# Optimization experiments

Hardware: AMD Instinct MI355X
Metric: run time of the kernel (lower is better)

The kernel has to match this reference:

```python
import jax, jax.numpy as jnp
import numpy as np

B, N, CIN, K, HID = 16, 4096, 64, 64, 128
RATIO, RADIUS = 0.25, 0.2
S = int(N * RATIO)  # 1024 sampled centers per cloud


def setup_inputs() -> dict:
    key = jax.random.key(0)
    k1, k2, k3, k4 = jax.random.split(key, 4)
    x = jax.random.normal(k1, (B * N, CIN), jnp.float32)
    pos = jax.random.uniform(k2, (B * N, 3), jnp.float32)  # unit cube
    batch = jnp.repeat(jnp.arange(B, dtype=jnp.int32), N)  # sorted cloud ids
    W1 = jax.random.normal(k3, (CIN + 3, HID), jnp.float32) / np.sqrt(CIN + 3)
    b1 = jnp.zeros((HID,), jnp.float32)
    W2 = jax.random.normal(k4, (HID, HID), jnp.float32) / np.sqrt(HID)
    b2 = jnp.zeros((HID,), jnp.float32)
    return {"x": x, "pos": pos, "batch": batch, "W1": W1, "b1": b1, "W2": W2, "b2": b2}


def _fps(pos_b):
    """Farthest point sampling on one cloud [N,3] -> S int32 indices (start=0, deterministic)."""
    def step(carry, _):
        min_d, last = carry
        d = jnp.sum((pos_b - pos_b[last]) ** 2, axis=-1)  # [N]
        min_d = jnp.minimum(min_d, d)
        nxt = jnp.argmax(min_d).astype(jnp.int32)
        return (min_d, nxt), last
    init = (jnp.full((N,), jnp.inf, pos_b.dtype), jnp.int32(0))
    _, idx = jax.lax.scan(step, init, None, length=S)
    return idx  # [S]


def _forward(x, pos, W1, b1, W2, b2):
    xb = x.reshape(B, N, CIN)
    pb = pos.reshape(B, N, 3)
    idx = jax.vmap(_fps)(pb)  # [B,S]
    centers = jnp.take_along_axis(pb, idx[:, :, None], axis=1)  # [B,S,3]
    # ball query: squared dists centers->all points of same cloud
    d2 = jnp.sum((centers[:, :, None, :] - pb[:, None, :, :]) ** 2, axis=-1)  # [B,S,N]
    masked = jnp.where(d2 <= RADIUS * RADIUS, d2, jnp.inf)
    negv, nbr = jax.lax.top_k(-masked, K)  # K nearest within radius; [B,S,K]
    valid = negv > -jnp.inf  # [B,S,K]
    gather = jax.vmap(lambda a, i: a[i])
    x_j = gather(xb, nbr)  # [B,S,K,CIN]
    p_j = gather(pb, nbr)  # [B,S,K,3]
    rel = p_j - centers[:, :, None, :]
    h = jnp.concatenate([x_j, rel], axis=-1)  # [B,S,K,CIN+3]
    h = jax.nn.relu(h @ W1 + b1)
    h = jax.nn.relu(h @ W2 + b2)  # local_nn message
    h = jnp.where(valid[..., None], h, -jnp.inf)
    out = jnp.max(h, axis=2)  # max-aggregation over neighbors -> [B,S,HID]
    return out.reshape(B * S, HID), centers.reshape(B * S, 3)


def reference(x, pos, batch, W1, b1, W2, b2):
    out, pos_out = _forward(x, pos, W1, b1, W2, b2)
    batch_out = jnp.repeat(jnp.arange(B, dtype=jnp.int32), S)
    return out, pos_out, batch_out
```

## Files before the change

### kernel.cpp

```cpp
#include <hip/hip_runtime.h>
#include <cstdint>
#include <cstddef>

#define BB   16
#define NN   4096
#define CINN 64
#define KKK  64
#define HIDD 128
#define SSS  1024
#define MAXC 320
#define NCH  2
#define CHS  512

typedef __attribute__((ext_vector_type(8))) short short8;
typedef __attribute__((ext_vector_type(4))) float f32x4;
typedef unsigned long long u64;

__device__ __forceinline__ float d2_exact(float ax, float ay, float az,
                                          float bx, float by, float bz) {
  float dx = __fsub_rn(ax, bx);
  float dy = __fsub_rn(ay, by);
  float dz = __fsub_rn(az, bz);
  return __fadd_rn(__fadd_rn(__fmul_rn(dx, dx), __fmul_rn(dy, dy)), __fmul_rn(dz, dz));
}

__device__ __forceinline__ unsigned short f2bf(float f) {
  unsigned u = __float_as_uint(f);
  return (unsigned short)((u + 0x7fffu + ((u >> 16) & 1u)) >> 16);
}

__device__ __forceinline__ void fps_role(int chunk, int bid, int tid,
                                         const float* __restrict__ pos,
                                         int* __restrict__ fps_idx,
                                         float* __restrict__ md_ws,
                                         int* __restrict__ last_ws,
                                         float* __restrict__ pos_out,
                                         float* __restrict__ batch_out,
                                         char* smem) {
  __builtin_amdgcn_s_setprio(3);
  float* px = (float*)smem;
  float* py = px + NN;
  float* pz = py + NN;
  u64* slots = (u64*)(pz + NN);
  int* sel = (int*)(slots + 8);
  const float* pb = pos + (size_t)bid * NN * 3;
  for (int i = tid; i < NN; i += 256) {
    px[i] = pb[3 * i + 0];
    py[i] = pb[3 * i + 1];
    pz[i] = pb[3 * i + 2];
  }
  if (chunk == 0) {
    #pragma unroll
    for (int kk = 0; kk < 4; ++kk)
      batch_out[bid * SSS + kk * 256 + tid] = (float)bid;
  }
  __syncthreads();

  float qx[16], qy[16], qz[16], md[16];
  #pragma unroll
  for (int j = 0; j < 16; ++j) {
    const int i = j * 256 + tid;
    qx[j] = px[i]; qy[j] = py[i]; qz[j] = pz[i];
    asm volatile("" : "+v"(qx[j]), "+v"(qy[j]), "+v"(qz[j]));
    md[j] = __builtin_inff();
  }
  int last, tb;
  const int cbase = chunk * CHS;
  const int te = cbase + CHS;
  if (chunk == 0) {
    last = 0; tb = 1;
    if (tid == 0) {
      fps_idx[bid * SSS] = 0;
      pos_out[(size_t)bid * SSS * 3 + 0] = px[0];
      pos_out[(size_t)bid * SSS * 3 + 1] = py[0];
      pos_out[(size_t)bid * SSS * 3 + 2] = pz[0];
    }
  } else {
    #pragma unroll
    for (int j = 0; j < 16; ++j) md[j] = md_ws[bid * 4096 + j * 256 + tid];
    last = last_ws[bid]; tb = cbase;
  }

  for (int t = tb; t < te; ++t) {
    const float lx = px[last], ly = py[last], lz = pz[last];
    float bv = -1.f;
    int bj = 0;
    #pragma unroll
    for (int j = 0; j < 16; ++j) {
      const float d = d2_exact(qx[j], qy[j], qz[j], lx, ly, lz);
      md[j] = fminf(md[j], d);
      if (md[j] > bv) { bv = md[j]; bj = j; }
    }
    unsigned klo = ~(unsigned)(bj * 256 + tid);
    unsigned khi = __float_as_uint(bv);
#define FPS_DPP_STAGE(CTRL, RMASK)                                                            \
    {                                                                                          \
      unsigned slo = (unsigned)__builtin_amdgcn_update_dpp(0, (int)klo, CTRL, RMASK, 0xf, true); \
      unsigned shi = (unsigned)__builtin_amdgcn_update_dpp(0, (int)khi, CTRL, RMASK, 0xf, true); \
      if ((((u64)shi << 32) | slo) > (((u64)khi << 32) | klo)) { khi = shi; klo = slo; }       \
    }
    FPS_DPP_STAGE(0x111, 0xf)
    FPS_DPP_STAGE(0x112, 0xf)
    FPS_DPP_STAGE(0x114, 0xf)
    FPS_DPP_STAGE(0x118, 0xf)
    FPS_DPP_STAGE(0x142, 0xa)
    FPS_DPP_STAGE(0x143, 0xc)
#undef FPS_DPP_STAGE
    u64* sl = slots + (t & 1) * 4;
    if ((tid & 63) == 63) sl[tid >> 6] = ((u64)khi << 32) | klo;
    __syncthreads();
    u64 mm = sl[0];
    #pragma unroll
    for (int w = 1; w < 4; ++w) mm = sl[w] > mm ? sl[w] : mm;
    last = (int)(~(unsigned)(mm & 0xffffffffull));
    if (tid == 0) sel[t - cbase] = last;
  }

  __syncthreads();
  for (int e = tid; e < CHS; e += 256) {
    const int t2 = cbase + e;
    if (t2 == 0) continue;
    const int idx = sel[e];
    fps_idx[bid * SSS + t2] = idx;
    pos_out[((size_t)bid * SSS + t2) * 3 + 0] = px[idx];
    pos_out[((size_t)bid * SSS + t2) * 3 + 1] = py[idx];
    pos_out[((size_t)bid * SSS + t2) * 3 + 2] = pz[idx];
  }
  if (chunk == 0) {
    #pragma unroll
    for (int j = 0; j < 16; ++j) md_ws[bid * 4096 + j * 256 + tid] = md[j];
    if (tid == 0) last_ws[bid] = last;
  }
}

__device__ __forceinline__ void y1_role(int j, int tid,
                                        const float* __restrict__ x,
                                        const float* __restrict__ W1,
                                        unsigned short* __restrict__ y1,
                                        char* smem) {
  float* sW = (float*)smem;
  float* sx = (float*)(smem + 32768);
  const int cloud = ((j >> 12) << 3) | (j & 7);
  const int local = (j >> 3) & 511;
  const int p0 = cloud * NN + local * 8;
  for (int e = tid; e < CINN * HIDD; e += 256) sW[e] = W1[e];
  for (int e = tid; e < 8 * CINN; e += 256) sx[e] = x[(size_t)p0 * CINN + e];
  __syncthreads();
  const int h = tid & 127;
  const int pg = (tid >> 7) * 4;
  float a0 = 0.f, a1 = 0.f, a2 = 0.f, a3 = 0.f;
  for (int c = 0; c < CINN; ++c) {
    const float w = sW[c * HIDD + h];
    a0 = fmaf(sx[(pg + 0) * CINN + c], w, a0);
    a1 = fmaf(sx[(pg + 1) * CINN + c], w, a1);
    a2 = fmaf(sx[(pg + 2) * CINN + c], w, a2);
    a3 = fmaf(sx[(pg + 3) * CINN + c], w, a3);
  }
  y1[(size_t)(p0 + pg + 0) * HIDD + h] = f2bf(a0);
  y1[(size_t)(p0 + pg + 1) * HIDD + h] = f2bf(a1);
  y1[(size_t)(p0 + pg + 2) * HIDD + h] = f2bf(a2);
  y1[(size_t)(p0 + pg + 3) * HIDD + h] = f2bf(a3);
}

__device__ __forceinline__ void bq_role(int cc, int i, int tid,
                                        const float* __restrict__ pos,
                                        const int* __restrict__ fps_idx,
                                        int* __restrict__ nbr,
                                        int* __restrict__ cnt,
                                        char* smem) {
  const int b = i >> 6;
  const int t0 = cc * CHS + (i & 63) * 8;
  const int gbase = b * SSS + t0;
  float* cd = (float*)smem;
  int*   ci = (int*)(smem + 10240);
  int*   ctr = (int*)(smem + 20480);
  int*   scn = ctr + 8;
  float* cctr = (float*)(scn + 8);

  const float* pb = pos + (size_t)b * NN * 3;
  if (tid < 8) { ctr[tid] = 0; scn[tid] = 0; }
  if (tid < 8) {
    const int cp = fps_idx[gbase + tid];
    cctr[tid * 3 + 0] = pb[cp * 3 + 0];
    cctr[tid * 3 + 1] = pb[cp * 3 + 1];
    cctr[tid * 3 + 2] = pb[cp * 3 + 2];
  }
  __syncthreads();
  float cx[8], cy[8], cz[8];
  #pragma unroll
  for (int c = 0; c < 8; ++c) {
    cx[c] = cctr[c * 3 + 0]; cy[c] = cctr[c * 3 + 1]; cz[c] = cctr[c * 3 + 2];
  }
  #pragma unroll 4
  for (int s2 = 0; s2 < 16; ++s2) {
    const int p = s2 * 256 + tid;
    const float x = pb[3 * p + 0], y = pb[3 * p + 1], z = pb[3 * p + 2];
    #pragma unroll
    for (int c = 0; c < 8; ++c) {
      const float d2 = d2_exact(x, y, z, cx[c], cy[c], cz[c]);
      if (d2 <= 0.04f) {
        const int slot = atomicAdd(&ctr[c], 1);
        if (slot < MAXC) { cd[c * MAXC + slot] = d2; ci[c * MAXC + slot] = p; }
      }
    }
  }
  __syncthreads();
  #pragma unroll 1
  for (int c = 0; c < 8; ++c) {
    const int C = min(ctr[c], MAXC);
    for (int j = tid; j < C; j += 256) {
      const float dj = cd[c * MAXC + j];
      const int ij = ci[c * MAXC + j];
      int rank = 0;
      for (int m = 0; m < C; ++m) {
        const float dm = cd[c * MAXC + m];
        const int im = ci[c * MAXC + m];
        rank += (dm < dj || (dm == dj && im < ij)) ? 1 : 0;
      }
      if (rank < KKK) nbr[(size_t)(gbase + c) * KKK + atomicAdd(&scn[c], 1)] = ij;
    }
  }
  __syncthreads();
  if (tid < 8) cnt[gbase + tid] = scn[tid];
}

__device__ __forceinline__ void mlp_role(int cc, int m, int tid,
                                         const float* __restrict__ pos,
                                         const unsigned short* __restrict__ y1,
                                         const float* __restrict__ W1,
                                         const float* __restrict__ b1,
                                         const unsigned short* __restrict__ W2t,
                                         const float* __restrict__ b2,
                                         const int* __restrict__ fps_idx,
                                         const int* __restrict__ nbr,
                                         const int* __restrict__ cnt,
                                         float* __restrict__ out,
                                         char* smem) {
  const int b = ((m >> 11) << 3) | (m & 7);
  const int loc = (m >> 3) & 255;
  const int g0 = b * SSS + cc * CHS + loc * 2;
  char* Hb = smem;
  float* s_ctr = (float*)(smem + 32768);
  int* s_M = (int*)(smem + 32800);
  int* s_pidx = (int*)(smem + 32832);
  float* s_rel = (float*)(smem + 33344);

  const int wv = tid >> 6, ln = tid & 63;
  const int mw = wv >> 1, nw = wv & 1;
  const int lr = ln & 15, lg = ln >> 4;

  if (tid < 2) {
    s_M[tid] = min(cnt[g0 + tid], KKK);
    const int cp = fps_idx[g0 + tid];
    s_ctr[tid * 3 + 0] = pos[((size_t)b * NN + cp) * 3 + 0];
    s_ctr[tid * 3 + 1] = pos[((size_t)b * NN + cp) * 3 + 1];
    s_ctr[tid * 3 + 2] = pos[((size_t)b * NN + cp) * 3 + 2];
  }
  __syncthreads();

  if (tid < 128) {
    const int ci = tid >> 6, k = tid & 63;
    int p = -1;
    float rx = 0.f, ry = 0.f, rz = 0.f;
    if (k < s_M[ci]) {
      p = nbr[(size_t)(g0 + ci) * KKK + k];
      rx = pos[((size_t)b * NN + p) * 3 + 0] - s_ctr[ci * 3 + 0];
      ry = pos[((size_t)b * NN + p) * 3 + 1] - s_ctr[ci * 3 + 1];
      rz = pos[((size_t)b * NN + p) * 3 + 2] - s_ctr[ci * 3 + 2];
    }
    s_pidx[tid] = p;
    s_rel[tid * 3 + 0] = rx; s_rel[tid * 3 + 1] = ry; s_rel[tid * 3 + 2] = rz;
  }
  __syncthreads();

  const float2 b1v = *(const float2*)(b1 + ln * 2);
  const float2 wav = *(const float2*)(W1 + 64 * HIDD + ln * 2);
  const float2 wbv = *(const float2*)(W1 + 65 * HIDD + ln * 2);
  const float2 wcv = *(const float2*)(W1 + 66 * HIDD + ln * 2);
  const int rbase = wv * 32;
  #pragma unroll
  for (int qb = 0; qb < 4; ++qb) {
    unsigned yreg[8];
    #pragma unroll
    for (int rr = 0; rr < 8; ++rr) {
      const int p = s_pidx[rbase + qb * 8 + rr];
      const int pa = p < 0 ? 0 : p;
      yreg[rr] = *(const unsigned*)(y1 + ((size_t)(b * NN + pa)) * HIDD + ln * 2);
    }
    #pragma unroll
    for (int rr = 0; rr < 8; ++rr) {
      const int r = rbase + qb * 8 + rr;
      const int p = s_pidx[r];
      unsigned val = 0u;
      if (p >= 0) {
        const float rx = s_rel[r * 3 + 0], ry = s_rel[r * 3 + 1], rz = s_rel[r * 3 + 2];
        const float y0 = __uint_as_float(yreg[rr] << 16);
        const float y1f = __uint_as_float(yreg[rr] & 0xffff0000u);
        const float v0 = fmaxf(y0 + b1v.x + rx * wav.x + ry * wbv.x + rz * wcv.x, 0.f);
        const float v1 = fmaxf(y1f + b1v.y + rx * wav.y + ry * wbv.y + rz * wcv.y, 0.f);
        val = (unsigned)f2bf(v0) | ((unsigned)f2bf(v1) << 16);
      }
      *(unsigned*)(Hb + r * 256 + ((ln * 4) ^ ((r & 7) << 4))) = val;
    }
  }
  __syncthreads();

  f32x4 zero = {0.f, 0.f, 0.f, 0.f};
  f32x4 acc[4][4];
  #pragma unroll
  for (int mi = 0; mi < 4; ++mi)
    #pragma unroll
    for (int ni = 0; ni < 4; ++ni) acc[mi][ni] = zero;

  #pragma unroll
  for (int ks = 0; ks < 4; ++ks) {
    short8 bfr[4];
    #pragma unroll
    for (int ni = 0; ni < 4; ++ni)
      bfr[ni] = *(const short8*)(W2t + (size_t)(nw * 64 + ni * 16 + lr) * HIDD + ks * 32 + lg * 8);
    short8 af[4];
    #pragma unroll
    for (int mi = 0; mi < 4; ++mi) {
      const int row = mw * 64 + mi * 16 + lr;
      af[mi] = *(const short8*)(Hb + row * 256 + ((ks * 64 + lg * 16) ^ ((row & 7) << 4)));
    }
    #pragma unroll
    for (int mi = 0; mi < 4; ++mi)
      #pragma unroll
      for (int ni = 0; ni < 4; ++ni)
        acc[mi][ni] = __builtin_amdgcn_mfma_f32_16x16x32_bf16(af[mi], bfr[ni], acc[mi][ni], 0, 0, 0);
  }

  const int cId = g0 + mw;
  const int Mc = s_M[mw];
  #pragma unroll
  for (int ni = 0; ni < 4; ++ni) {
    const float b2v = b2[nw * 64 + ni * 16 + lr];
    float cm = 0.f;
    #pragma unroll
    for (int mi = 0; mi < 4; ++mi)
      #pragma unroll
      for (int rr = 0; rr < 4; ++rr) {
        const int k = mi * 16 + lg * 4 + rr;
        const float v = fmaxf(acc[mi][ni][rr] + b2v, 0.f);
        cm = fmaxf(cm, k < Mc ? v : 0.f);
      }
    cm = fmaxf(cm, __shfl_xor(cm, 16, 64));
    cm = fmaxf(cm, __shfl_xor(cm, 32, 64));
    if (ln < 16) out[(size_t)cId * HIDD + nw * 64 + ni * 16 + lr] = cm;
  }
}

__global__ __launch_bounds__(256) void k_phase0(const float* __restrict__ x,
                                                const float* __restrict__ pos,
                                                const float* __restrict__ W1,
                                                const float* __restrict__ W2,
                                                unsigned short* __restrict__ W2t,
                                                int* __restrict__ fps_idx,
                                                unsigned short* __restrict__ y1,
                                                float* __restrict__ md_ws,
                                                int* __restrict__ last_ws,
                                                float* __restrict__ pos_out,
                                                float* __restrict__ batch_out) {
  __shared__ __align__(16) char smem[51264];
  const int bid = blockIdx.x, tid = threadIdx.x;
  if (bid < BB) {
    fps_role(0, bid, tid, pos, fps_idx, md_ws, last_ws, pos_out, batch_out, smem);
  } else if (bid < 16 + 8192) {
    y1_role(bid - 16, tid, x, W1, y1, smem);
  } else {
    for (int e = tid; e < HIDD * HIDD; e += 256) {
      const int n = e >> 7, hh = e & 127;
      W2t[e] = f2bf(W2[hh * HIDD + n]);
    }
  }
}

__global__ __launch_bounds__(256) void k_phase1(const float* __restrict__ pos,
                                                int* __restrict__ fps_idx,
                                                int* __restrict__ cnt,
                                                int* __restrict__ nbr,
                                                float* __restrict__ md_ws,
                                                int* __restrict__ last_ws,
                                                float* __restrict__ pos_out,
                                                float* __restrict__ batch_out) {
  __shared__ __align__(16) char smem[51264];
  const int bid = blockIdx.x, tid = threadIdx.x;
  if (bid < BB) {
    fps_role(1, bid, tid, pos, fps_idx, md_ws, last_ws, pos_out, batch_out, smem);
  } else {
    bq_role(0, bid - 16, tid, pos, fps_idx, nbr, cnt, smem);
  }
}

__global__ __launch_bounds__(256) void k_phase2(const float* __restrict__ pos,
                                                const int* __restrict__ fps_idx,
                                                int* __restrict__ nbr,
                                                int* __restrict__ cnt) {
  __shared__ __align__(16) char smem[20736];
  bq_role(1, blockIdx.x, threadIdx.x, pos, fps_idx, nbr, cnt, smem);
}

__global__ __launch_bounds__(256) void k_phase3(const float* __restrict__ pos,
                                                const unsigned short* __restrict__ y1,
                                                const float* __restrict__ W1,
                                                const float* __restrict__ b1,
                                                const unsigned short* __restrict__ W2t,
                                                const float* __restrict__ b2,
                                                const int* __restrict__ fps_idx,
                                                const int* __restrict__ nbr,
                                                const int* __restrict__ cnt,
                                                float* __restrict__ out) {
  __shared__ __align__(16) char smem[34944];
  const int bid = blockIdx.x;
  mlp_role(bid >> 12, bid & 4095, threadIdx.x, pos, y1, W1, b1, W2t, b2,
           fps_idx, nbr, cnt, out, smem);
}

extern "C" void kernel_launch(void* const* d_in, const int* in_sizes, int n_in,
                              void* d_out, int out_size, void* d_ws, size_t ws_size,
                              hipStream_t stream) {
  const float* x   = (const float*)d_in[0];
  const float* pos = (const float*)d_in[1];
  const float* W1  = (const float*)d_in[3];
  const float* b1  = (const float*)d_in[4];
  const float* W2  = (const float*)d_in[5];
  const float* b2  = (const float*)d_in[6];

  float* out       = (float*)d_out;
  float* pos_out   = out + (size_t)BB * SSS * HIDD;
  float* batch_out = pos_out + (size_t)BB * SSS * 3;

  int* fps_idx        = (int*)d_ws;
  int* cnt            = (int*)((char*)d_ws + 65536);
  unsigned short* W2t = (unsigned short*)((char*)d_ws + 131072);
  int* last_ws        = (int*)((char*)d_ws + 163840);
  int* nbr            = (int*)((char*)d_ws + 262144);
  unsigned short* y1  = (unsigned short*)((char*)d_ws + 262144 + 4194304);
  float* md_ws        = (float*)((char*)d_ws + 262144 + 4194304 + 33554432);

  k_phase0<<<16 + 8192 + 1, 256, 0, stream>>>(x, pos, W1, W2, W2t, fps_idx, y1,
                                              md_ws, last_ws, pos_out, batch_out);
  k_phase1<<<16 + 1024, 256, 0, stream>>>(pos, fps_idx, cnt, nbr,
                                          md_ws, last_ws, pos_out, batch_out);
  k_phase2<<<1024, 256, 0, stream>>>(pos, fps_idx, nbr, cnt);
  k_phase3<<<8192, 256, 0, stream>>>(pos, y1, W1, b1, W2t, b2,
                                     fps_idx, nbr, cnt, out);
}
```

Measured before the change: 821.5 us.

## Pack two FPS clouds per 512-thread block and widen y1/ball-query blocks

Farthest-point sampling now runs two clouds per 512-thread block, each half on its own shared-memory region. The y1 projection blocks grow to 512 threads covering 32 points each, which cuts block count and W1 reloads. The ball-query role is templated on thread count so phase 1 can use 512-thread blocks. This trades fewer FPS CUs and wider barriers on the latency-bound FPS loop for less per-block overhead elsewhere. The risk is that two FPS waves per SIMD, sharing a block-wide barrier, slow down the serial critical path.

```diff
diff --git a/kernel.cpp b/kernel.cpp
--- a/kernel.cpp
+++ b/kernel.cpp
@@ -11,6 +11,7 @@
 #define MAXC 320
 #define NCH  2
 #define CHS  512
+#define FPSB 51264
 
 typedef __attribute__((ext_vector_type(8))) short short8;
 typedef __attribute__((ext_vector_type(4))) float f32x4;
@@ -29,7 +30,7 @@
   return (unsigned short)((u + 0x7fffu + ((u >> 16) & 1u)) >> 16);
 }
 
-__device__ __forceinline__ void fps_role(int chunk, int bid, int tid,
+__device__ __forceinline__ void fps_role(int chunk, int cloud, int tid,
                                          const float* __restrict__ pos,
                                          int* __restrict__ fps_idx,
                                          float* __restrict__ md_ws,
@@ -43,7 +44,7 @@
   float* pz = py + NN;
   u64* slots = (u64*)(pz + NN);
   int* sel = (int*)(slots + 8);
-  const float* pb = pos + (size_t)bid * NN * 3;
+  const float* pb = pos + (size_t)cloud * NN * 3;
   for (int i = tid; i < NN; i += 256) {
     px[i] = pb[3 * i + 0];
     py[i] = pb[3 * i + 1];
@@ -52,7 +53,7 @@
   if (chunk == 0) {
     #pragma unroll
     for (int kk = 0; kk < 4; ++kk)
-      batch_out[bid * SSS + kk * 256 + tid] = (float)bid;
+      batch_out[cloud * SSS + kk * 256 + tid] = (float)cloud;
   }
   __syncthreads();
 
@@ -70,15 +71,15 @@
   if (chunk == 0) {
     last = 0; tb = 1;
     if (tid == 0) {
-      fps_idx[bid * SSS] = 0;
-      pos_out[(size_t)bid * SSS * 3 + 0] = px[0];
-      pos_out[(size_t)bid * SSS * 3 + 1] = py[0];
-      pos_out[(size_t)bid * SSS * 3 + 2] = pz[0];
+      fps_idx[cloud * SSS] = 0;
+      pos_out[(size_t)cloud * SSS * 3 + 0] = px[0];
+      pos_out[(size_t)cloud * SSS * 3 + 1] = py[0];
+      pos_out[(size_t)cloud * SSS * 3 + 2] = pz[0];
     }
   } else {
     #pragma unroll
-    for (int j = 0; j < 16; ++j) md[j] = md_ws[bid * 4096 + j * 256 + tid];
-    last = last_ws[bid]; tb = cbase;
+    for (int j = 0; j < 16; ++j) md[j] = md_ws[cloud * 4096 + j * 256 + tid];
+    last = last_ws[cloud]; tb = cbase;
   }
 
   for (int t = tb; t < te; ++t) {
@@ -121,15 +122,15 @@
     const int t2 = cbase + e;
     if (t2 == 0) continue;
     const int idx = sel[e];
-    fps_idx[bid * SSS + t2] = idx;
-    pos_out[((size_t)bid * SSS + t2) * 3 + 0] = px[idx];
-    pos_out[((size_t)bid * SSS + t2) * 3 + 1] = py[idx];
-    pos_out[((size_t)bid * SSS + t2) * 3 + 2] = pz[idx];
+    fps_idx[cloud * SSS + t2] = idx;
+    pos_out[((size_t)cloud * SSS + t2) * 3 + 0] = px[idx];
+    pos_out[((size_t)cloud * SSS + t2) * 3 + 1] = py[idx];
+    pos_out[((size_t)cloud * SSS + t2) * 3 + 2] = pz[idx];
   }
   if (chunk == 0) {
     #pragma unroll
-    for (int j = 0; j < 16; ++j) md_ws[bid * 4096 + j * 256 + tid] = md[j];
-    if (tid == 0) last_ws[bid] = last;
+    for (int j = 0; j < 16; ++j) md_ws[cloud * 4096 + j * 256 + tid] = md[j];
+    if (tid == 0) last_ws[cloud] = last;
   }
 }
 
@@ -140,28 +141,28 @@
                                         char* smem) {
   float* sW = (float*)smem;
   float* sx = (float*)(smem + 32768);
-  const int cloud = ((j >> 12) << 3) | (j & 7);
-  const int local = (j >> 3) & 511;
-  const int p0 = cloud * NN + local * 8;
-  for (int e = tid; e < CINN * HIDD; e += 256) sW[e] = W1[e];
-  for (int e = tid; e < 8 * CINN; e += 256) sx[e] = x[(size_t)p0 * CINN + e];
+  const int cloud = ((j >> 10) << 3) | (j & 7);
+  const int local = (j >> 3) & 127;
+  const int p0 = cloud * NN + local * 32;
+  for (int e = tid; e < CINN * HIDD; e += 512) sW[e] = W1[e];
+  for (int e = tid; e < 32 * CINN; e += 512) sx[e] = x[(size_t)p0 * CINN + e];
   __syncthreads();
   const int h = tid & 127;
-  const int pg = (tid >> 7) * 4;
-  float a0 = 0.f, a1 = 0.f, a2 = 0.f, a3 = 0.f;
+  const int pg = (tid >> 7) * 8;
+  float a[8];
+  #pragma unroll
+  for (int k = 0; k < 8; ++k) a[k] = 0.f;
   for (int c = 0; c < CINN; ++c) {
     const float w = sW[c * HIDD + h];
-    a0 = fmaf(sx[(pg + 0) * CINN + c], w, a0);
-    a1 = fmaf(sx[(pg + 1) * CINN + c], w, a1);
-    a2 = fmaf(sx[(pg + 2) * CINN + c], w, a2);
-    a3 = fmaf(sx[(pg + 3) * CINN + c], w, a3);
-  }
-  y1[(size_t)(p0 + pg + 0) * HIDD + h] = f2bf(a0);
-  y1[(size_t)(p0 + pg + 1) * HIDD + h] = f2bf(a1);
-  y1[(size_t)(p0 + pg + 2) * HIDD + h] = f2bf(a2);
-  y1[(size_t)(p0 + pg + 3) * HIDD + h] = f2bf(a3);
-}
-
+    #pragma unroll
+    for (int k = 0; k < 8; ++k) a[k] = fmaf(sx[(pg + k) * CINN + c], w, a[k]);
+  }
+  #pragma unroll
+  for (int k = 0; k < 8; ++k)
+    y1[(size_t)(p0 + pg + k) * HIDD + h] = f2bf(a[k]);
+}
+
+template <int NT>
 __device__ __forceinline__ void bq_role(int cc, int i, int tid,
                                         const float* __restrict__ pos,
                                         const int* __restrict__ fps_idx,
@@ -192,8 +193,7 @@
     cx[c] = cctr[c * 3 + 0]; cy[c] = cctr[c * 3 + 1]; cz[c] = cctr[c * 3 + 2];
   }
   #pragma unroll 4
-  for (int s2 = 0; s2 < 16; ++s2) {
-    const int p = s2 * 256 + tid;
+  for (int p = tid; p < NN; p += NT) {
     const float x = pb[3 * p + 0], y = pb[3 * p + 1], z = pb[3 * p + 2];
     #pragma unroll
     for (int c = 0; c < 8; ++c) {
@@ -208,7 +208,7 @@
   #pragma unroll 1
   for (int c = 0; c < 8; ++c) {
     const int C = min(ctr[c], MAXC);
-    for (int j = tid; j < C; j += 256) {
+    for (int j = tid; j < C; j += NT) {
       const float dj = cd[c * MAXC + j];
       const int ij = ci[c * MAXC + j];
       int rank = 0;
@@ -351,7 +351,7 @@
   }
 }
 
-__global__ __launch_bounds__(256) void k_phase0(const float* __restrict__ x,
+__global__ __launch_bounds__(512) void k_phase0(const float* __restrict__ x,
                                                 const float* __restrict__ pos,
                                                 const float* __restrict__ W1,
                                                 const float* __restrict__ W2,
@@ -362,21 +362,23 @@
                                                 int* __restrict__ last_ws,
                                                 float* __restrict__ pos_out,
                                                 float* __restrict__ batch_out) {
-  __shared__ __align__(16) char smem[51264];
+  __shared__ __align__(16) char smem[2 * FPSB];
   const int bid = blockIdx.x, tid = threadIdx.x;
-  if (bid < BB) {
-    fps_role(0, bid, tid, pos, fps_idx, md_ws, last_ws, pos_out, batch_out, smem);
-  } else if (bid < 16 + 8192) {
-    y1_role(bid - 16, tid, x, W1, y1, smem);
+  if (bid < 8) {
+    const int half = tid >> 8, lt = tid & 255;
+    fps_role(0, bid * 2 + half, lt, pos, fps_idx, md_ws, last_ws, pos_out, batch_out,
+             smem + half * FPSB);
+  } else if (bid < 8 + 2048) {
+    y1_role(bid - 8, tid, x, W1, y1, smem);
   } else {
-    for (int e = tid; e < HIDD * HIDD; e += 256) {
+    for (int e = tid; e < HIDD * HIDD; e += 512) {
       const int n = e >> 7, hh = e & 127;
       W2t[e] = f2bf(W2[hh * HIDD + n]);
     }
   }
 }
 
-__global__ __launch_bounds__(256) void k_phase1(const float* __restrict__ pos,
+__global__ __launch_bounds__(512) void k_phase1(const float* __restrict__ pos,
                                                 int* __restrict__ fps_idx,
                                                 int* __restrict__ cnt,
                                                 int* __restrict__ nbr,
@@ -384,12 +386,14 @@
                                                 int* __restrict__ last_ws,
                                                 float* __restrict__ pos_out,
                                                 float* __restrict__ batch_out) {
-  __shared__ __align__(16) char smem[51264];
+  __shared__ __align__(16) char smem[2 * FPSB];
   const int bid = blockIdx.x, tid = threadIdx.x;
-  if (bid < BB) {
-    fps_role(1, bid, tid, pos, fps_idx, md_ws, last_ws, pos_out, batch_out, smem);
+  if (bid < 8) {
+    const int half = tid >> 8, lt = tid & 255;
+    fps_role(1, bid * 2 + half, lt, pos, fps_idx, md_ws, last_ws, pos_out, batch_out,
+             smem + half * FPSB);
   } else {
-    bq_role(0, bid - 16, tid, pos, fps_idx, nbr, cnt, smem);
+    bq_role<512>(0, bid - 8, tid, pos, fps_idx, nbr, cnt, smem);
   }
 }
 
@@ -398,7 +402,7 @@
                                                 int* __restrict__ nbr,
                                                 int* __restrict__ cnt) {
   __shared__ __align__(16) char smem[20736];
-  bq_role(1, blockIdx.x, threadIdx.x, pos, fps_idx, nbr, cnt, smem);
+  bq_role<256>(1, blockIdx.x, threadIdx.x, pos, fps_idx, nbr, cnt, smem);
 }
 
 __global__ __launch_bounds__(256) void k_phase3(const float* __restrict__ pos,
@@ -439,10 +443,10 @@
   unsigned short* y1  = (unsigned short*)((char*)d_ws + 262144 + 4194304);
   float* md_ws        = (float*)((char*)d_ws + 262144 + 4194304 + 33554432);
 
-  k_phase0<<<16 + 8192 + 1, 256, 0, stream>>>(x, pos, W1, W2, W2t, fps_idx, y1,
-                                              md_ws, last_ws, pos_out, batch_out);
-  k_phase1<<<16 + 1024, 256, 0, stream>>>(pos, fps_idx, cnt, nbr,
-                                          md_ws, last_ws, pos_out, batch_out);
+  k_phase0<<<8 + 2048 + 1, 512, 0, stream>>>(x, pos, W1, W2, W2t, fps_idx, y1,
+                                             md_ws, last_ws, pos_out, batch_out);
+  k_phase1<<<8 + 1024, 512, 0, stream>>>(pos, fps_idx, cnt, nbr,
+                                         md_ws, last_ws, pos_out, batch_out);
   k_phase2<<<1024, 256, 0, stream>>>(pos, fps_idx, nbr, cnt);
   k_phase3<<<8192, 256, 0, stream>>>(pos, y1, W1, b1, W2t, b2,
                                      fps_idx, nbr, cnt, out);
```

After: 1.129 ms. +37.4%, slower.

## Speed FPS loop with tree argmax and broadcast coords; overlap MLP chunk with ball query

Applied to the files above, without the earlier changes.

The FPS inner loop now finds the per-thread max with a tree reduction and a match mask instead of a serial compare chain. The winning wave lane also writes its point coordinates to shared memory, so the next iteration no longer needs a dependent LDS lookup px[last]. Separately, the first MLP chunk is moved into the phase-2 launch alongside the second ball-query chunk, so those two pieces of work overlap. The cost is slightly more shared memory per block and a larger phase-2 kernel footprint, since it now sizes shared memory for the MLP.

```diff
diff --git a/kernel.cpp b/kernel.cpp
--- a/kernel.cpp
+++ b/kernel.cpp
@@ -41,8 +41,9 @@
   float* px = (float*)smem;
   float* py = px + NN;
   float* pz = py + NN;
-  u64* slots = (u64*)(pz + NN);
-  int* sel = (int*)(slots + 8);
+  u64* skey = (u64*)(pz + NN);
+  float* scd = (float*)(skey + 8);
+  int* sel = (int*)(scd + 32);
   const float* pb = pos + (size_t)bid * NN * 3;
   for (int i = tid; i < NN; i += 256) {
     px[i] = pb[3 * i + 0];
@@ -67,32 +68,41 @@
   int last, tb;
   const int cbase = chunk * CHS;
   const int te = cbase + CHS;
+  float cxr, cyr, czr;
   if (chunk == 0) {
     last = 0; tb = 1;
+    cxr = px[0]; cyr = py[0]; czr = pz[0];
     if (tid == 0) {
       fps_idx[bid * SSS] = 0;
-      pos_out[(size_t)bid * SSS * 3 + 0] = px[0];
-      pos_out[(size_t)bid * SSS * 3 + 1] = py[0];
-      pos_out[(size_t)bid * SSS * 3 + 2] = pz[0];
+      pos_out[(size_t)bid * SSS * 3 + 0] = cxr;
+      pos_out[(size_t)bid * SSS * 3 + 1] = cyr;
+      pos_out[(size_t)bid * SSS * 3 + 2] = czr;
     }
   } else {
     #pragma unroll
     for (int j = 0; j < 16; ++j) md[j] = md_ws[bid * 4096 + j * 256 + tid];
     last = last_ws[bid]; tb = cbase;
+    cxr = px[last]; cyr = py[last]; czr = pz[last];
   }
 
   for (int t = tb; t < te; ++t) {
-    const float lx = px[last], ly = py[last], lz = pz[last];
-    float bv = -1.f;
-    int bj = 0;
-    #pragma unroll
-    for (int j = 0; j < 16; ++j) {
-      const float d = d2_exact(qx[j], qy[j], qz[j], lx, ly, lz);
-      md[j] = fminf(md[j], d);
-      if (md[j] > bv) { bv = md[j]; bj = j; }
-    }
-    unsigned klo = ~(unsigned)(bj * 256 + tid);
-    unsigned khi = __float_as_uint(bv);
+    #pragma unroll
+    for (int j = 0; j < 16; ++j)
+      md[j] = fminf(md[j], d2_exact(qx[j], qy[j], qz[j], cxr, cyr, czr));
+    float t8[8], t4[4], t2[2];
+    #pragma unroll
+    for (int j = 0; j < 8; ++j) t8[j] = fmaxf(md[j], md[j + 8]);
+    #pragma unroll
+    for (int j = 0; j < 4; ++j) t4[j] = fmaxf(t8[j], t8[j + 4]);
+    t2[0] = fmaxf(t4[0], t4[2]); t2[1] = fmaxf(t4[1], t4[3]);
+    const float bv = fmaxf(t2[0], t2[1]);
+    unsigned mask = 0u;
+    #pragma unroll
+    for (int j = 0; j < 16; ++j) mask |= (md[j] == bv) ? (1u << j) : 0u;
+    const int bj = __builtin_ctz(mask);
+    const unsigned myklo = ~(unsigned)(bj * 256 + tid);
+    const unsigned mykhi = __float_as_uint(bv);
+    unsigned klo = myklo, khi = mykhi;
 #define FPS_DPP_STAGE(CTRL, RMASK)                                                            \
     {                                                                                          \
       unsigned slo = (unsigned)__builtin_amdgcn_update_dpp(0, (int)klo, CTRL, RMASK, 0xf, true); \
@@ -106,13 +116,32 @@
     FPS_DPP_STAGE(0x142, 0xa)
     FPS_DPP_STAGE(0x143, 0xc)
 #undef FPS_DPP_STAGE
-    u64* sl = slots + (t & 1) * 4;
-    if ((tid & 63) == 63) sl[tid >> 6] = ((u64)khi << 32) | klo;
+    const unsigned wlo = (unsigned)__builtin_amdgcn_readlane((int)klo, 63);
+    const unsigned whi = (unsigned)__builtin_amdgcn_readlane((int)khi, 63);
+    const int par = (t & 1) * 4;
+    if (myklo == wlo && mykhi == whi) {
+      const int w = par + (tid >> 6);
+      skey[w] = ((u64)whi << 32) | wlo;
+      scd[w * 4 + 0] = qx[bj];
+      scd[w * 4 + 1] = qy[bj];
+      scd[w * 4 + 2] = qz[bj];
+    }
     __syncthreads();
-    u64 mm = sl[0];
-    #pragma unroll
-    for (int w = 1; w < 4; ++w) mm = sl[w] > mm ? sl[w] : mm;
-    last = (int)(~(unsigned)(mm & 0xffffffffull));
+    const u64 k0 = skey[par + 0], k1 = skey[par + 1], k2 = skey[par + 2], k3 = skey[par + 3];
+    const float a0x = scd[(par + 0) * 4], a0y = scd[(par + 0) * 4 + 1], a0z = scd[(par + 0) * 4 + 2];
+    const float a1x = scd[(par + 1) * 4], a1y = scd[(par + 1) * 4 + 1], a1z = scd[(par + 1) * 4 + 2];
+    const float a2x = scd[(par + 2) * 4], a2y = scd[(par + 2) * 4 + 1], a2z = scd[(par + 2) * 4 + 2];
+    const float a3x = scd[(par + 3) * 4], a3y = scd[(par + 3) * 4 + 1], a3z = scd[(par + 3) * 4 + 2];
+    const bool s01 = k1 > k0;
+    const u64 ka = s01 ? k1 : k0;
+    const float bx0 = s01 ? a1x : a0x, by0 = s01 ? a1y : a0y, bz0 = s01 ? a1z : a0z;
+    const bool s23 = k3 > k2;
+    const u64 kb = s23 ? k3 : k2;
+    const float bx1 = s23 ? a3x : a2x, by1 = s23 ? a3y : a2y, bz1 = s23 ? a3z : a2z;
+    const bool sab = kb > ka;
+    const u64 win = sab ? kb : ka;
+    cxr = sab ? bx1 : bx0; cyr = sab ? by1 : by0; czr = sab ? bz1 : bz0;
+    last = (int)(~(unsigned)(win & 0xffffffffull));
     if (tid == 0) sel[t - cbase] = last;
   }
 
@@ -362,7 +391,7 @@
                                                 int* __restrict__ last_ws,
                                                 float* __restrict__ pos_out,
                                                 float* __restrict__ batch_out) {
-  __shared__ __align__(16) char smem[51264];
+  __shared__ __align__(16) char smem[51392];
   const int bid = blockIdx.x, tid = threadIdx.x;
   if (bid < BB) {
     fps_role(0, bid, tid, pos, fps_idx, md_ws, last_ws, pos_out, batch_out, smem);
@@ -384,7 +413,7 @@
                                                 int* __restrict__ last_ws,
                                                 float* __restrict__ pos_out,
                                                 float* __restrict__ batch_out) {
-  __shared__ __align__(16) char smem[51264];
+  __shared__ __align__(16) char smem[51392];
   const int bid = blockIdx.x, tid = threadIdx.x;
   if (bid < BB) {
     fps_role(1, bid, tid, pos, fps_idx, md_ws, last_ws, pos_out, batch_out, smem);
@@ -394,11 +423,22 @@
 }
 
 __global__ __launch_bounds__(256) void k_phase2(const float* __restrict__ pos,
-                                                const int* __restrict__ fps_idx,
+                                                const unsigned short* __restrict__ y1,
+                                                const float* __restrict__ W1,
+                                                const float* __restrict__ b1,
+                                                const unsigned short* __restrict__ W2t,
+                                                const float* __restrict__ b2,
+                                                int* __restrict__ fps_idx,
                                                 int* __restrict__ nbr,
-                                                int* __restrict__ cnt) {
-  __shared__ __align__(16) char smem[20736];
-  bq_role(1, blockIdx.x, threadIdx.x, pos, fps_idx, nbr, cnt, smem);
+                                                int* __restrict__ cnt,
+                                                float* __restrict__ out) {
+  __shared__ __align__(16) char smem[34944];
+  const int bid = blockIdx.x, tid = threadIdx.x;
+  if (bid < 1024) {
+    bq_role(1, bid, tid, pos, fps_idx, nbr, cnt, smem);
+  } else {
+    mlp_role(0, bid - 1024, tid, pos, y1, W1, b1, W2t, b2, fps_idx, nbr, cnt, out, smem);
+  }
 }
 
 __global__ __launch_bounds__(256) void k_phase3(const float* __restrict__ pos,
@@ -412,8 +452,7 @@
                                                 const int* __restrict__ cnt,
                                                 float* __restrict__ out) {
   __shared__ __align__(16) char smem[34944];
-  const int bid = blockIdx.x;
-  mlp_role(bid >> 12, bid & 4095, threadIdx.x, pos, y1, W1, b1, W2t, b2,
+  mlp_role(1, blockIdx.x, threadIdx.x, pos, y1, W1, b1, W2t, b2,
            fps_idx, nbr, cnt, out, smem);
 }
 
@@ -443,7 +482,8 @@
                                               md_ws, last_ws, pos_out, batch_out);
   k_phase1<<<16 + 1024, 256, 0, stream>>>(pos, fps_idx, cnt, nbr,
                                           md_ws, last_ws, pos_out, batch_out);
-  k_phase2<<<1024, 256, 0, stream>>>(pos, fps_idx, nbr, cnt);
-  k_phase3<<<8192, 256, 0, stream>>>(pos, y1, W1, b1, W2t, b2,
+  k_phase2<<<1024 + 4096, 256, 0, stream>>>(pos, y1, W1, b1, W2t, b2,
+                                            fps_idx, nbr, cnt, out);
+  k_phase3<<<4096, 256, 0, stream>>>(pos, y1, W1, b1, W2t, b2,
                                      fps_idx, nbr, cnt, out);
 }
```

Result: slower. 1.092 ms (+32.9%).
